# Performance work log

Measured on AMD Instinct MI355X. Metric: run time of the kernel, lower is better.

## Reference

```python
import jax, jax.numpy as jnp
import numpy as np

N_HEADS = 16


def setup_inputs() -> dict:
    key = jax.random.key(0)
    k1, k2, k3 = jax.random.split(key, 3)
    B, S, D = 2, 2048, 1024
    x = jax.random.normal(k1, (B, S, D), dtype=jnp.float32)
    # causal mask: 1 = keep, 0 = masked (module does masked_fill(mask == 0, -inf))
    mask = jnp.broadcast_to(jnp.tril(jnp.ones((S, S), dtype=jnp.int32)), (B, S, S))
    # torch Linear(bias=False) weights, stored transposed so y = x @ W
    w_qkv = jax.random.normal(k2, (D, 3 * D), dtype=jnp.float32) * (1.0 / np.sqrt(D))
    w_out = jax.random.normal(k3, (D, D), dtype=jnp.float32) * (1.0 / np.sqrt(D))
    return {"x": x, "mask": mask, "w_qkv": w_qkv, "w_out": w_out}


def reference(x, mask, w_qkv, w_out):
    B, S, D = x.shape
    H = N_HEADS
    dh = D // H
    scale = 1.0 / np.sqrt(dh)

    qkv = x @ w_qkv                                   # [B,S,3D]
    qkv = qkv.reshape(B, S, 3, H, dh)
    qkv = jnp.transpose(qkv, (2, 0, 3, 1, 4))         # [3,B,H,S,dh]
    q, k, v = qkv[0], qkv[1], qkv[2]

    scores = jnp.einsum("bhqd,bhkd->bhqk", q, k) * scale   # [B,H,S,S]
    scores = jnp.where(mask[:, None, :, :] == 0, -jnp.inf, scores)
    attn = jax.nn.softmax(scores, axis=-1)            # dropout = identity (eval)

    out = jnp.einsum("bhqk,bhkd->bhqd", attn, v)      # [B,H,S,dh]
    out = jnp.transpose(out, (0, 2, 1, 3)).reshape(B, S, D)
    return out @ w_out
```

## Files before the change

### kernel.cpp

```cpp
#include <hip/hip_runtime.h>

typedef unsigned short u16;
typedef unsigned int u32;
typedef u16 u16x8 __attribute__((ext_vector_type(8)));
typedef u16 u16x4 __attribute__((ext_vector_type(4)));
typedef u32 u32x4 __attribute__((ext_vector_type(4)));
typedef __bf16 bf16x8 __attribute__((ext_vector_type(8)));
typedef float f32x4 __attribute__((ext_vector_type(4)));
typedef float f32x16 __attribute__((ext_vector_type(16)));


static __device__ __forceinline__ u16 bf16_rn(float f) {
    union { float f; u32 u; } a; a.f = f;
    u32 u = a.u;
    return (u16)((u + 0x7FFFu + ((u >> 16) & 1u)) >> 16);
}

static __device__ __forceinline__ bf16x8 as_bf(u16x8 v) {
    return __builtin_bit_cast(bf16x8, v);
}

static __device__ __forceinline__ u32 cvt_pk_bf16(float lo, float hi) {
    u32 r;
    asm("v_cvt_pk_bf16_f32 %0, %1, %2" : "=v"(r) : "v"(lo), "v"(hi));
    return r;
}

static __device__ __forceinline__ void glds16(const u16* g, u16* lds) {
    __builtin_amdgcn_global_load_lds(
        (const __attribute__((address_space(1))) void*)g,
        (__attribute__((address_space(3))) void*)lds, 16, 0, 0);
}


__global__ void k_cvt(const float* __restrict__ src, u16* __restrict__ dst, int n8) {
    int i = blockIdx.x * blockDim.x + threadIdx.x;
    if (i >= n8) return;
    const float4* s = (const float4*)src + (size_t)i * 2;
    float4 a = s[0], b = s[1];
    u16x8 v;
    v[0] = bf16_rn(a.x); v[1] = bf16_rn(a.y); v[2] = bf16_rn(a.z); v[3] = bf16_rn(a.w);
    v[4] = bf16_rn(b.x); v[5] = bf16_rn(b.y); v[6] = bf16_rn(b.z); v[7] = bf16_rn(b.w);
    *(u16x8*)(dst + (size_t)i * 8) = v;
}


__global__ void k_tr_cvt(const float* __restrict__ src, u16* __restrict__ dst,
                         int R, int C) {
    __shared__ float t[32][33];
    const int bx = blockIdx.x * 32, by = blockIdx.y * 32;
    const int tx = threadIdx.x, ty = threadIdx.y;
#pragma unroll
    for (int j = 0; j < 32; j += 8)
        t[ty + j][tx] = src[(size_t)(by + ty + j) * C + bx + tx];
    __syncthreads();
#pragma unroll
    for (int j = 0; j < 32; j += 8)
        dst[(size_t)(bx + ty + j) * R + by + tx] = bf16_rn(t[tx][ty + j]);
}


template <int MODE>
__launch_bounds__(256, 2)
__global__ void k_gemm(const u16* __restrict__ A, const u16* __restrict__ Bt,
                       void* __restrict__ outp, int M, int N, int K) {
    __shared__ __align__(16) u16 As[2][128 * 32];
    __shared__ __align__(16) u16 Bs[2][128 * 32];
    const int tid = threadIdx.x;
    const int l = tid & 63, wv = tid >> 6;
    const int wr = wv >> 1, wc = wv & 1;
    const int l15 = l & 15, lg = l >> 4;
    const int m0 = blockIdx.y * 128, n0 = blockIdx.x * 128;
    const int NT = K >> 5;

    const f32x4 fzero = {0.f, 0.f, 0.f, 0.f};
    f32x4 acc[4][4];
#pragma unroll
    for (int m = 0; m < 4; m++)
#pragma unroll
        for (int n = 0; n < 4; n++) acc[m][n] = fzero;

    const int grow0 = wv * 32 + (l >> 2);
    const int gcol = (l & 3) * 8;

    auto stage = [&](int buf, int kt) {
        const size_t ko = (size_t)kt * 32 + gcol;
        glds16(A  + (size_t)(m0 + grow0) * K + ko,      &As[buf][wv * 1024]);
        glds16(A  + (size_t)(m0 + grow0 + 16) * K + ko, &As[buf][wv * 1024 + 512]);
        glds16(Bt + (size_t)(n0 + grow0) * K + ko,      &Bs[buf][wv * 1024]);
        glds16(Bt + (size_t)(n0 + grow0 + 16) * K + ko, &Bs[buf][wv * 1024 + 512]);
    };

    stage(0, 0);
    int cur = 0;
    for (int kt = 0; kt < NT; ++kt) {
        if (kt + 1 < NT) {
            stage(cur ^ 1, kt + 1);
            asm volatile("s_waitcnt vmcnt(4)" ::: "memory");
        } else {
            asm volatile("s_waitcnt vmcnt(0)" ::: "memory");
        }
        __builtin_amdgcn_s_barrier();
        u16x8 af[4], bfv[4];
#pragma unroll
        for (int m = 0; m < 4; m++)
            af[m] = *(const u16x8*)(&As[cur][(wr * 64 + m * 16 + l15) * 32 + lg * 8]);
#pragma unroll
        for (int n = 0; n < 4; n++)
            bfv[n] = *(const u16x8*)(&Bs[cur][(wc * 64 + n * 16 + l15) * 32 + lg * 8]);
#pragma unroll
        for (int m = 0; m < 4; m++)
#pragma unroll
            for (int n = 0; n < 4; n++)
                acc[m][n] = __builtin_amdgcn_mfma_f32_16x16x32_bf16(
                    as_bf(af[m]), as_bf(bfv[n]), acc[m][n], 0, 0, 0);
        __builtin_amdgcn_s_barrier();
        cur ^= 1;
    }

    if (MODE == 0) {
        u16* qkv = (u16*)outp;
#pragma unroll
        for (int m = 0; m < 4; m++) {
            const int rb = m0 + wr * 64 + m * 16 + lg * 4;
#pragma unroll
            for (int n = 0; n < 4; n++) {
                const int c = n0 + wc * 64 + n * 16;
                const int t = c >> 10, h = (c >> 6) & 15, d0 = (c & 63) + l15;
                const float scl = (t == 0) ? 0.18033688011112042f : 1.0f;
#pragma unroll
                for (int i = 0; i < 4; i++) {
                    const int r = rb + i;
                    const int b = r >> 11, s = r & 2047;
                    qkv[((((size_t)t * 2 + b) * 16 + h) * 2048 + s) * 64 + d0] =
                        bf16_rn(acc[m][n][i] * scl);
                }
            }
        }
    } else {
        float* O = (float*)outp;
#pragma unroll
        for (int m = 0; m < 4; m++) {
            const int rb = m0 + wr * 64 + m * 16 + lg * 4;
#pragma unroll
            for (int n = 0; n < 4; n++) {
                const int c = n0 + wc * 64 + n * 16 + l15;
#pragma unroll
                for (int i = 0; i < 4; i++)
                    O[(size_t)(rb + i) * N + c] = acc[m][n][i];
            }
        }
    }
}


__launch_bounds__(256, 2)
__global__ void k_attn(const u16* __restrict__ qkv, u16* __restrict__ ab) {
    __shared__ __align__(16) char arena[4][9216];
    __shared__ float MLs[4][64];
    const int tid = threadIdx.x, l = tid & 63, wv = tid >> 6;
    const int q = l & 31, h = l >> 5;
    const int bid = blockIdx.x;
    const int bh = bid & 31;
    const int pp = bid >> 5;
    const int b = bh >> 4, hd = bh & 15;
    const size_t plane = (size_t)2048 * 64;
    const u16* Qg = qkv + ((size_t)(0 + b) * 16 + hd) * plane;
    const u16* Kg = qkv + ((size_t)(2 + b) * 16 + hd) * plane;
    const u16* Vg = qkv + ((size_t)(4 + b) * 16 + hd) * plane;
    u16* VT = (u16*)arena[wv];

    const int g = l & 7, qd = l >> 3;
    const u16* Kbase = Kg + (size_t)q * 64 + 8 * h;
    const u16* Vbase = Vg + (size_t)(8 * qd) * 64 + 8 * g;
    const int Fq0 = 8 * (q >> 3) + ((q & 7) ^ ((q >> 3) & 7));
    const int d1 = q + 32;
    const int Fq1 = 8 * (d1 >> 3) + ((d1 & 7) ^ ((d1 >> 3) & 7));
    const u16* vr0 = VT + Fq0 * 72 + 8 * h;
    const u16* vr1 = VT + Fq1 * 72 + 8 * h;
    const float FIXM = 12.0f;

    for (int ph = 0; ph < 2; ++ph) {
        const int qt = ph ? 63 - pp : pp;
        const int q0 = qt * 32, qg = q0 + q;
        const int n64 = (qt >> 1) + 1;

        u16x8 qf[4];
#pragma unroll
        for (int s = 0; s < 4; ++s)
            qf[s] = *(const u16x8*)(Qg + (size_t)(q0 + q) * 64 + s * 16 + 8 * h);

        f32x16 oacc0 = 0, oacc1 = 0;
        float l_run = 0.f;

        u16x8 vK[8], vV[8];
        if (wv < n64) {
#pragma unroll
            for (int s = 0; s < 4; ++s) {
                vK[s]     = *(const u16x8*)(Kbase + (size_t)(wv * 64) * 64 + s * 16);
                vK[4 + s] = *(const u16x8*)(Kbase + (size_t)(wv * 64 + 32) * 64 + s * 16);
            }
#pragma unroll
            for (int j = 0; j < 8; ++j)
                vV[j] = *(const u16x8*)(Vbase + (size_t)(wv * 64 + j) * 64);
        }

        for (int t = wv; t < n64; t += 4) {
            const int kv0 = t * 64;
            f32x16 sa = 0, sb = 0;
            __builtin_amdgcn_s_setprio(1);
#pragma unroll
            for (int s = 0; s < 4; ++s)
                sa = __builtin_amdgcn_mfma_f32_32x32x16_bf16(as_bf(vK[s]), as_bf(qf[s]), sa, 0, 0, 0);
#pragma unroll
            for (int s = 0; s < 4; ++s)
                sb = __builtin_amdgcn_mfma_f32_32x32x16_bf16(as_bf(vK[4 + s]), as_bf(qf[s]), sb, 0, 0, 0);
            __builtin_amdgcn_s_setprio(0);
#pragma unroll
            for (int j = 0; j < 8; ++j) {
                u16x8 col;
#pragma unroll
                for (int r = 0; r < 8; ++r) col[r] = vV[r][j];
                *(u16x8*)(VT + (size_t)(8 * g + (j ^ g)) * 72 + 8 * qd) = col;
            }
            if (t + 4 < n64) {
#pragma unroll
                for (int s = 0; s < 4; ++s) {
                    vK[s]     = *(const u16x8*)(Kbase + (size_t)((t + 4) * 64) * 64 + s * 16);
                    vK[4 + s] = *(const u16x8*)(Kbase + (size_t)((t + 4) * 64 + 32) * 64 + s * 16);
                }
#pragma unroll
                for (int j = 0; j < 8; ++j)
                    vV[j] = *(const u16x8*)(Vbase + (size_t)((t + 4) * 64 + j) * 64);
            }
            if (t == n64 - 1) {
#pragma unroll
                for (int r = 0; r < 16; ++r) {
                    const int kg = kv0 + (r & 3) + 8 * (r >> 2) + 4 * h;
                    if (kg > qg) sa[r] = -__builtin_inff();
                    if (kg + 32 > qg) sb[r] = -__builtin_inff();
                }
            }
#pragma unroll
            for (int r = 0; r < 16; ++r) sa[r] = exp2f(sa[r] - FIXM);
#pragma unroll
            for (int r = 0; r < 16; ++r) sb[r] = exp2f(sb[r] - FIXM);
            float ts[8];
#pragma unroll
            for (int i = 0; i < 8; ++i)
                ts[i] = (sa[i] + sa[i + 8]) + (sb[i] + sb[i + 8]);
#pragma unroll
            for (int i = 0; i < 4; ++i) ts[i] += ts[i + 4];
            l_run += (ts[0] + ts[2]) + (ts[1] + ts[3]);
            u32 pk[16];
#pragma unroll
            for (int i = 0; i < 8; ++i) pk[i]     = cvt_pk_bf16(sa[2 * i], sa[2 * i + 1]);
#pragma unroll
            for (int i = 0; i < 8; ++i) pk[8 + i] = cvt_pk_bf16(sb[2 * i], sb[2 * i + 1]);
#pragma unroll
            for (int ks = 0; ks < 4; ++ks) {
                const int base = (ks >> 1) * 8 + 4 * (ks & 1);
                u32 w0 = pk[base],     w1 = pk[base + 1];
                u32 w2 = pk[base + 2], w3 = pk[base + 3];
                asm("v_permlane32_swap_b32 %0, %1" : "+v"(w0), "+v"(w2));
                asm("v_permlane32_swap_b32 %0, %1" : "+v"(w1), "+v"(w3));
                const u16x8 pb = __builtin_bit_cast(u16x8, (u32x4){w0, w1, w2, w3});
                const u16x8 va0 = *(const u16x8*)(vr0 + ks * 16);
                const u16x8 va1 = *(const u16x8*)(vr1 + ks * 16);
                __builtin_amdgcn_s_setprio(1);
                oacc0 = __builtin_amdgcn_mfma_f32_32x32x16_bf16(as_bf(va0), as_bf(pb), oacc0, 0, 0, 0);
                oacc1 = __builtin_amdgcn_mfma_f32_32x32x16_bf16(as_bf(va1), as_bf(pb), oacc1, 0, 0, 0);
                __builtin_amdgcn_s_setprio(0);
            }
        }
        asm volatile("" ::: "memory");
        float* Op = (float*)arena[wv];
#pragma unroll
        for (int r = 0; r < 16; ++r) {
            const int dr = (r & 3) + 8 * (r >> 2) + 4 * h;
            Op[q * 64 + ((dr + 2 * q) & 63)]      = oacc0[r];
            Op[q * 64 + ((dr + 32 + 2 * q) & 63)] = oacc1[r];
        }
        MLs[wv][l] = l_run;
        __syncthreads();
        const int tq = tid >> 3, dblk = (tid & 7) * 8;
        float L = 0.f;
#pragma unroll
        for (int w = 0; w < 4; ++w) L += MLs[w][tq] + MLs[w][32 + tq];
        const float inv = 1.f / L;
        u16x8 outv;
#pragma unroll
        for (int j = 0; j < 8; ++j) {
            const int d = dblk + j;
            float acc = 0.f;
#pragma unroll
            for (int w = 0; w < 4; ++w)
                acc += ((const float*)arena[w])[tq * 64 + ((d + 2 * tq) & 63)];
            outv[j] = bf16_rn(acc * inv);
        }
        *(u16x8*)(ab + (size_t)(b * 2048 + q0 + tq) * 1024 + hd * 64 + dblk) = outv;
        __syncthreads();
    }
}


extern "C" void kernel_launch(void* const* d_in, const int* in_sizes, int n_in,
                              void* d_out, int out_size, void* d_ws, size_t ws_size,
                              hipStream_t stream) {
    const float* x     = (const float*)d_in[0];
    const float* w_qkv = (const float*)d_in[2];
    const float* w_out = (const float*)d_in[3];
    float* out = (float*)d_out;
    u16* ws = (u16*)d_ws;

    u16* xb    = ws;
    u16* wqkvT = ws + 4194304;
    u16* woutT = ws + 7340032;
    u16* qkvb  = ws + 8388608;
    u16* abuf  = ws;

    k_cvt<<<2048, 256, 0, stream>>>(x, xb, 524288);
    k_tr_cvt<<<dim3(96, 32), dim3(32, 8), 0, stream>>>(w_qkv, wqkvT, 1024, 3072);
    k_tr_cvt<<<dim3(32, 32), dim3(32, 8), 0, stream>>>(w_out, woutT, 1024, 1024);
    k_gemm<0><<<dim3(24, 32), 256, 0, stream>>>(xb, wqkvT, qkvb, 4096, 3072, 1024);
    k_attn<<<1024, 256, 0, stream>>>(qkvb, abuf);
    k_gemm<1><<<dim3(8, 32), 256, 0, stream>>>(abuf, woutT, out, 4096, 1024, 1024);
}
```

Measured before the change: 127.8 us.

## Use 256x256-tile swizzled-LDS GEMM kernel for QKV projection

Adds a dedicated QKV projection kernel with 256x256 output tiles, 512 threads (8 waves, 128x64 per wave) and a K step of 64 split into two 32-wide LDS stages, with a double-buffered direct global-to-LDS prefetch. The LDS layout is XOR-swizzled to avoid bank conflicts, and MFMA issue is raised with s_setprio. The aim is more data reuse per loaded byte and better latency hiding than the 128x128 kernel. The trade-off is only 192 blocks, fewer than two waves' worth on a 256-CU part, plus much higher register and LDS pressure. The output GEMM keeps the old kernel, now specialised to fp32 output.

```diff
diff --git a/kernel.cpp b/kernel.cpp
--- a/kernel.cpp
+++ b/kernel.cpp
@@ -60,10 +60,103 @@
 }
 
 
-template <int MODE>
+__launch_bounds__(512, 1)
+__global__ void k_gemm256(const u16* __restrict__ A, const u16* __restrict__ Bt,
+                          u16* __restrict__ qkv, int M, int N, int K) {
+    __shared__ __align__(16) u16 As[2][2][256 * 32];
+    __shared__ __align__(16) u16 Bs[2][2][256 * 32];
+    const int tid = threadIdx.x;
+    const int l = tid & 63, wv = tid >> 6;
+    const int wr = wv >> 2, wc = wv & 3;
+    const int l15 = l & 15, lg = l >> 4;
+    const int m0 = blockIdx.y * 256, n0 = blockIdx.x * 256;
+    const int NT = K >> 6;
+
+    const f32x4 fzero = {0.f, 0.f, 0.f, 0.f};
+    f32x4 acc[8][4];
+#pragma unroll
+    for (int m = 0; m < 8; m++)
+#pragma unroll
+        for (int n = 0; n < 4; n++) acc[m][n] = fzero;
+
+    const int lr = l >> 2;
+    const int lc = (((l & 3) ^ ((l >> 3) & 3))) * 8;
+
+    auto stage = [&](int buf, int kt, int ks) {
+#pragma unroll
+        for (int j = 0; j < 2; ++j) {
+            const int rbase = j * 128 + wv * 16;
+            const size_t gco = (size_t)kt * 64 + ks * 32 + lc;
+            glds16(A  + (size_t)(m0 + rbase + lr) * K + gco, &As[buf][ks][rbase * 32]);
+            glds16(Bt + (size_t)(n0 + rbase + lr) * K + gco, &Bs[buf][ks][rbase * 32]);
+        }
+    };
+
+    stage(0, 0, 0);
+    stage(0, 0, 1);
+    asm volatile("s_waitcnt vmcnt(0)" ::: "memory");
+    __builtin_amdgcn_s_barrier();
+
+    int cur = 0;
+    for (int kt = 0; kt < NT; ++kt) {
+        const bool more = (kt + 1 < NT);
+#pragma unroll
+        for (int ks = 0; ks < 2; ++ks) {
+            if (ks == 0) {
+                asm volatile("s_waitcnt vmcnt(4)" ::: "memory");
+            } else if (more) {
+                asm volatile("s_waitcnt vmcnt(4)" ::: "memory");
+            } else {
+                asm volatile("s_waitcnt vmcnt(0)" ::: "memory");
+            }
+            __builtin_amdgcn_s_barrier();
+            if (more) stage(cur ^ 1, kt + 1, ks);
+            u16x8 bfv[4], af[8];
+#pragma unroll
+            for (int n = 0; n < 4; ++n) {
+                const int row = wc * 64 + n * 16 + l15;
+                bfv[n] = *(const u16x8*)(&Bs[cur][ks][row * 32 + ((lg ^ ((row >> 1) & 3)) * 8)]);
+            }
+#pragma unroll
+            for (int m = 0; m < 8; ++m) {
+                const int row = wr * 128 + m * 16 + l15;
+                af[m] = *(const u16x8*)(&As[cur][ks][row * 32 + ((lg ^ ((row >> 1) & 3)) * 8)]);
+            }
+            __builtin_amdgcn_s_setprio(1);
+#pragma unroll
+            for (int m = 0; m < 8; ++m)
+#pragma unroll
+                for (int n = 0; n < 4; ++n)
+                    acc[m][n] = __builtin_amdgcn_mfma_f32_16x16x32_bf16(
+                        as_bf(af[m]), as_bf(bfv[n]), acc[m][n], 0, 0, 0);
+            __builtin_amdgcn_s_setprio(0);
+        }
+        cur ^= 1;
+    }
+
+#pragma unroll
+    for (int m = 0; m < 8; m++) {
+        const int rb = m0 + wr * 128 + m * 16 + lg * 4;
+#pragma unroll
+        for (int n = 0; n < 4; n++) {
+            const int c = n0 + wc * 64 + n * 16;
+            const int t = c >> 10, h = (c >> 6) & 15, d0 = (c & 63) + l15;
+            const float scl = (t == 0) ? 0.18033688011112042f : 1.0f;
+#pragma unroll
+            for (int i = 0; i < 4; i++) {
+                const int r = rb + i;
+                const int b = r >> 11, s = r & 2047;
+                qkv[((((size_t)t * 2 + b) * 16 + h) * 2048 + s) * 64 + d0] =
+                    bf16_rn(acc[m][n][i] * scl);
+            }
+        }
+    }
+}
+
+
 __launch_bounds__(256, 2)
 __global__ void k_gemm(const u16* __restrict__ A, const u16* __restrict__ Bt,
-                       void* __restrict__ outp, int M, int N, int K) {
+                       float* __restrict__ O, int M, int N, int K) {
     __shared__ __align__(16) u16 As[2][128 * 32];
     __shared__ __align__(16) u16 Bs[2][128 * 32];
     const int tid = threadIdx.x;
@@ -118,37 +211,15 @@
         cur ^= 1;
     }
 
-    if (MODE == 0) {
-        u16* qkv = (u16*)outp;
-#pragma unroll
-        for (int m = 0; m < 4; m++) {
-            const int rb = m0 + wr * 64 + m * 16 + lg * 4;
-#pragma unroll
-            for (int n = 0; n < 4; n++) {
-                const int c = n0 + wc * 64 + n * 16;
-                const int t = c >> 10, h = (c >> 6) & 15, d0 = (c & 63) + l15;
-                const float scl = (t == 0) ? 0.18033688011112042f : 1.0f;
-#pragma unroll
-                for (int i = 0; i < 4; i++) {
-                    const int r = rb + i;
-                    const int b = r >> 11, s = r & 2047;
-                    qkv[((((size_t)t * 2 + b) * 16 + h) * 2048 + s) * 64 + d0] =
-                        bf16_rn(acc[m][n][i] * scl);
-                }
-            }
-        }
-    } else {
-        float* O = (float*)outp;
-#pragma unroll
-        for (int m = 0; m < 4; m++) {
-            const int rb = m0 + wr * 64 + m * 16 + lg * 4;
-#pragma unroll
-            for (int n = 0; n < 4; n++) {
-                const int c = n0 + wc * 64 + n * 16 + l15;
-#pragma unroll
-                for (int i = 0; i < 4; i++)
-                    O[(size_t)(rb + i) * N + c] = acc[m][n][i];
-            }
+#pragma unroll
+    for (int m = 0; m < 4; m++) {
+        const int rb = m0 + wr * 64 + m * 16 + lg * 4;
+#pragma unroll
+        for (int n = 0; n < 4; n++) {
+            const int c = n0 + wc * 64 + n * 16 + l15;
+#pragma unroll
+            for (int i = 0; i < 4; i++)
+                O[(size_t)(rb + i) * N + c] = acc[m][n][i];
         }
     }
 }
@@ -322,7 +393,7 @@
     k_cvt<<<2048, 256, 0, stream>>>(x, xb, 524288);
     k_tr_cvt<<<dim3(96, 32), dim3(32, 8), 0, stream>>>(w_qkv, wqkvT, 1024, 3072);
     k_tr_cvt<<<dim3(32, 32), dim3(32, 8), 0, stream>>>(w_out, woutT, 1024, 1024);
-    k_gemm<0><<<dim3(24, 32), 256, 0, stream>>>(xb, wqkvT, qkvb, 4096, 3072, 1024);
+    k_gemm256<<<dim3(12, 16), 512, 0, stream>>>(xb, wqkvT, qkvb, 4096, 3072, 1024);
     k_attn<<<1024, 256, 0, stream>>>(qkvb, abuf);
-    k_gemm<1><<<dim3(8, 32), 256, 0, stream>>>(abuf, woutT, out, 4096, 1024, 1024);
-}
+    k_gemm<<<dim3(8, 32), 256, 0, stream>>>(abuf, woutT, out, 4096, 1024, 1024);
+}
```

New measurement: 140.0 us. 1.1x slower.
